# Kernel optimization log

Hardware: AMD Instinct MI355X
Metric: run time of the kernel (lower is better)

Reference implementation:

```python
import jax, jax.numpy as jnp
import numpy as np

D = 8
W = 256
NUM_FREQS = 10
NUM_FREQS_VIEWS = 4
SKIPS = (4,)
PE_DIM = 3 + 2 * 3 * NUM_FREQS        # 63
VE_DIM = 3 + 2 * 3 * NUM_FREQS_VIEWS  # 27
N_RAYS, N_SAMPLES = 4096, 64


def embed(x, num_freqs):
    # torch order: [x, sin(x*f0), cos(x*f0), sin(x*f1), cos(x*f1), ...]
    freqs = (2.0 ** jnp.arange(num_freqs)).astype(x.dtype)
    xf = x[..., None, :] * freqs[:, None]              # [..., F, 3]
    sc = jnp.stack([jnp.sin(xf), jnp.cos(xf)], axis=-2)  # [..., F, 2, 3]
    return jnp.concatenate([x, sc.reshape(*x.shape[:-1], num_freqs * 6)], -1)


def setup_inputs() -> dict:
    key = jax.random.key(0)
    ks = iter(jax.random.split(key, 32))
    inp = {}
    inp["input_pts"] = jax.random.normal(next(ks), (N_RAYS, N_SAMPLES, 3), jnp.float32)
    inp["input_views"] = jax.random.normal(next(ks), (N_RAYS, 3), jnp.float32)
    # pts MLP: layer 5 (index 5) takes W + PE_DIM due to skip after layer 4
    in_dims = [PE_DIM] + [(W + PE_DIM) if i in SKIPS else W for i in range(D - 1)]
    for i, d in enumerate(in_dims):
        inp[f"pts_w{i}"] = jax.random.normal(next(ks), (d, W), jnp.float32) / np.sqrt(d).astype(np.float32)
        inp[f"pts_b{i}"] = jnp.zeros((W,), jnp.float32)
    inp["views_w"] = jax.random.normal(next(ks), (VE_DIM + W, W // 2), jnp.float32) / np.sqrt(VE_DIM + W).astype(np.float32)
    inp["views_b"] = jnp.zeros((W // 2,), jnp.float32)
    inp["feat_w"] = jax.random.normal(next(ks), (W, W), jnp.float32) / np.sqrt(W).astype(np.float32)
    inp["feat_b"] = jnp.zeros((W,), jnp.float32)
    inp["alpha_w"] = jax.random.normal(next(ks), (W, 1), jnp.float32) / np.sqrt(W).astype(np.float32)
    inp["alpha_b"] = jnp.zeros((1,), jnp.float32)
    inp["rgb_w"] = jax.random.normal(next(ks), (W // 2, 3), jnp.float32) / np.sqrt(W // 2).astype(np.float32)
    inp["rgb_b"] = jnp.zeros((3,), jnp.float32)
    return inp


def reference(input_pts, input_views,
              pts_w0, pts_b0, pts_w1, pts_b1, pts_w2, pts_b2, pts_w3, pts_b3,
              pts_w4, pts_b4, pts_w5, pts_b5, pts_w6, pts_b6, pts_w7, pts_b7,
              views_w, views_b, feat_w, feat_b, alpha_w, alpha_b, rgb_w, rgb_b):
    pts_ws = [pts_w0, pts_w1, pts_w2, pts_w3, pts_w4, pts_w5, pts_w6, pts_w7]
    pts_bs = [pts_b0, pts_b1, pts_b2, pts_b3, pts_b4, pts_b5, pts_b6, pts_b7]
    R, S = input_pts.shape[0], input_pts.shape[1]
    ep = embed(input_pts, NUM_FREQS).reshape(-1, PE_DIM)            # [R*S, 63]
    ev = embed(input_views, NUM_FREQS_VIEWS)                        # [R, 27]
    ev = jnp.broadcast_to(ev[:, None, :], (R, S, VE_DIM)).reshape(-1, VE_DIM)
    h = ep
    for i in range(D):
        h = jax.nn.relu(h @ pts_ws[i] + pts_bs[i])
        if i in SKIPS:
            h = jnp.concatenate([ep, h], -1)
    alpha = h @ alpha_w + alpha_b                                    # [R*S, 1]
    feature = h @ feat_w + feat_b                                    # [R*S, W]
    h2 = jax.nn.relu(jnp.concatenate([feature, ev], -1) @ views_w + views_b)
    rgb = h2 @ rgb_w + rgb_b                                         # [R*S, 3]
    return jnp.concatenate([rgb, alpha], -1).reshape(R, S, 4)
```

## Files before the change

kernel.cpp:

```cpp
#include <hip/hip_runtime.h>

typedef _Float16 h16;
typedef __attribute__((ext_vector_type(8))) _Float16 half8;
typedef __attribute__((ext_vector_type(4))) _Float16 half4;
typedef __attribute__((ext_vector_type(4))) float f32x4;
typedef __attribute__((ext_vector_type(16))) float f32x16;

#define LDH 264
#define LDE 72

constexpr size_t OFF_P0 = 0;
constexpr size_t OFF_P1 = 16384;
constexpr size_t OFF_P2 = 81920;
constexpr size_t OFF_P3 = 147456;
constexpr size_t OFF_P4 = 212992;
constexpr size_t OFF_P5 = 278528;
constexpr size_t OFF_P6 = 360448;
constexpr size_t OFF_P7 = 425984;
constexpr size_t OFF_FEAT = 491520;
constexpr size_t OFF_VIEWS = 557056;

__device__ __forceinline__ f32x16 mfma32(half8 a, half8 b, f32x16 c) {
  return __builtin_amdgcn_mfma_f32_32x32x16_f16(a, b, c, 0, 0, 0);
}

__device__ __forceinline__ half8 ldfrag(const h16* __restrict__ base, int frag, int l) {
  return *(const half8*)(base + (size_t)frag * 512 + (size_t)l * 8);
}

__global__ void convw_kernel(const float* __restrict__ src, h16* __restrict__ dst,
                             int Ksrc, int N, int Kp, int p, int npad, int rot) {
  int t = blockIdx.x * 256 + threadIdx.x;
  int nfrags = (Kp >> 4) * (N >> 5);
  int frag = t >> 6;
  if (frag >= nfrags) return;
  int l = t & 63;
  int ntiles = N >> 5;
  int kt = frag / ntiles;
  int nt = frag - kt * ntiles;
  int col = nt * 32 + (l & 31);
  int kbase = kt * 16 + (l >> 5) * 8;
  half8 v;
#pragma unroll
  for (int j = 0; j < 8; ++j) {
    int pr = kbase + j + rot;
    if (pr >= Kp) pr -= Kp;
    float x = 0.f;
    if (pr < p) {
      x = src[(size_t)pr * N + col];
    } else if (pr >= p + npad) {
      int r = pr - npad;
      if (r < Ksrc) x = src[(size_t)r * N + col];
    }
    v[j] = (h16)x;
  }
  *(half8*)(dst + (size_t)frag * 512 + (size_t)l * 8) = v;
}

struct Params {
  const float* pts;
  const float* views;
  const h16* wf;
  const float* pb[8];
  const float* views_b;
  const float* feat_b;
  const float* alpha_w;
  const float* alpha_b;
  const float* rgb_w;
  const float* rgb_b;
  float* out;
};

template <bool RELU>
__device__ __forceinline__ void epi(const f32x16& a0, const f32x16& a1,
                                    const float* __restrict__ bias,
                                    h16* __restrict__ Y, int w, int l, int lr) {
#pragma unroll
  for (int mt = 0; mt < 2; ++mt) {
    const f32x16& A = mt ? a1 : a0;
    int row = mt * 32 + lr;
#pragma unroll
    for (int g = 0; g < 4; ++g) {
      int n0 = w * 32 + g * 8 + ((l >> 5) * 4);
      f32x4 bv = *(const f32x4*)(bias + n0);
      half4 pk;
#pragma unroll
      for (int i = 0; i < 4; ++i) {
        float v = A[g * 4 + i] + bv[i];
        if (RELU) v = fmaxf(v, 0.f);
        pk[i] = (h16)v;
      }
      *(half4*)(Y + (size_t)row * LDH + n0) = pk;
    }
  }
}

template <bool RELU, bool EXTEP>
__device__ __forceinline__ void layer256(
    const h16* __restrict__ X, const h16* __restrict__ EPb, h16* __restrict__ Y,
    const h16* __restrict__ wcur, const h16* __restrict__ wnext,
    int nstride, int nbase, const float* __restrict__ bias,
    half8 (&bf)[8], half8 (&bt)[8], int w, int l, int lr, int lko) {
#pragma unroll
  for (int j = 0; j < 8; ++j) bt[j] = ldfrag(wcur, (8 + j) * 8 + w, l);
  half8 bep[4];
  f32x16 acc0 = (f32x16)0.f, acc1 = (f32x16)0.f;
#pragma unroll
  for (int kt = 0; kt < 16; ++kt) {
    half8 a = *(const half8*)(X + (size_t)lr * LDH + kt * 16 + lko);
    half8 b = kt < 8 ? bf[kt] : bt[kt - 8];
    acc0 = mfma32(b, a, acc0);
    if (EXTEP && kt == 7) {
#pragma unroll
      for (int j = 0; j < 4; ++j) bep[j] = ldfrag(wcur, (16 + j) * 8 + w, l);
    }
  }
  if (EXTEP) {
#pragma unroll
    for (int j = 0; j < 4; ++j) {
      half8 a = *(const half8*)(EPb + (size_t)lr * LDE + j * 16 + lko);
      acc0 = mfma32(bep[j], a, acc0);
    }
  }
#pragma unroll
  for (int kt = 0; kt < 16; ++kt) {
    half8 a = *(const half8*)(X + (size_t)(32 + lr) * LDH + kt * 16 + lko);
    half8 b = kt < 8 ? bf[kt] : bt[kt - 8];
    acc1 = mfma32(b, a, acc1);
    if (kt < 8) bf[kt] = ldfrag(wnext, kt * nstride + nbase, l);
  }
  if (EXTEP) {
#pragma unroll
    for (int j = 0; j < 4; ++j) {
      half8 a = *(const half8*)(EPb + (size_t)(32 + lr) * LDE + j * 16 + lko);
      acc1 = mfma32(bep[j], a, acc1);
    }
  }
  epi<RELU>(acc0, acc1, bias, Y, w, l, lr);
  __syncthreads();
}

__global__ __launch_bounds__(512, 4) void nerf_kernel(Params P) {
  __shared__ __align__(16) h16 ep[64 * LDE];
  __shared__ __align__(16) h16 h0[64 * LDH];
  __shared__ __align__(16) h16 h1[64 * LDH];
  __shared__ __align__(16) h16 evp[32];

  const int tid = threadIdx.x;
  const int w = tid >> 6, l = tid & 63;
  const int lr = l & 31;
  const int lko = (l >> 5) * 8;
  const int ray = blockIdx.x;
  const h16* wf = P.wf;

  half8 bt[8];
#pragma unroll
  for (int j = 0; j < 4; ++j) bt[j] = ldfrag(wf + OFF_P0, j * 8 + w, l);

  {
    const int s = tid >> 3, q = tid & 7;
    const float* ps = P.pts + ((size_t)ray * 64 + s) * 3;
    const float x0 = ps[0], x1 = ps[1], x2 = ps[2];
    half8 v;
#pragma unroll
    for (int j = 0; j < 8; ++j) {
      int p = q * 8 + j;
      float val;
      if (p < 3) {
        val = p == 0 ? x0 : (p == 1 ? x1 : x2);
      } else if (p < 63) {
        int t = p - 3;
        int f = t / 6, rem = t % 6, d = rem % 3;
        float x = (d == 0 ? x0 : (d == 1 ? x1 : x2)) * (float)(1 << f);
        val = (rem < 3) ? sinf(x) : cosf(x);
      } else {
        val = 0.f;
      }
      v[j] = (h16)val;
    }
    *(half8*)(ep + (size_t)s * LDE + q * 8) = v;
  }
  if (tid < 32) {
    const int idx = tid;
    float v = 0.f;
    if (idx < 27) {
      if (idx < 3) {
        v = P.views[(size_t)ray * 3 + idx];
      } else {
        const int f = (idx - 3) / 6, rem = (idx - 3) % 6, d = rem % 3;
        const float x = P.views[(size_t)ray * 3 + d] * (float)(1 << f);
        v = (rem < 3) ? sinf(x) : cosf(x);
      }
    }
    evp[idx] = (h16)v;
  }
  __syncthreads();

  half8 bf[8];

  {
    f32x16 acc0 = (f32x16)0.f, acc1 = (f32x16)0.f;
#pragma unroll
    for (int kt = 0; kt < 4; ++kt) {
      half8 a = *(const half8*)(ep + (size_t)lr * LDE + kt * 16 + lko);
      acc0 = mfma32(bt[kt], a, acc0);
    }
#pragma unroll
    for (int kt = 0; kt < 4; ++kt) {
      half8 a = *(const half8*)(ep + (size_t)(32 + lr) * LDE + kt * 16 + lko);
      acc1 = mfma32(bt[kt], a, acc1);
    }
#pragma unroll
    for (int j = 0; j < 8; ++j) bf[j] = ldfrag(wf + OFF_P1, j * 8 + w, l);
    epi<true>(acc0, acc1, P.pb[0], h0, w, l, lr);
    __syncthreads();
  }

  layer256<true, false>(h0, ep, h1, wf + OFF_P1, wf + OFF_P2, 8, w, P.pb[1], bf, bt, w, l, lr, lko);
  layer256<true, false>(h1, ep, h0, wf + OFF_P2, wf + OFF_P3, 8, w, P.pb[2], bf, bt, w, l, lr, lko);
  layer256<true, false>(h0, ep, h1, wf + OFF_P3, wf + OFF_P4, 8, w, P.pb[3], bf, bt, w, l, lr, lko);
  layer256<true, false>(h1, ep, h0, wf + OFF_P4, wf + OFF_P5, 8, w, P.pb[4], bf, bt, w, l, lr, lko);
  layer256<true, true>(h0, ep, h1, wf + OFF_P5, wf + OFF_P6, 8, w, P.pb[5], bf, bt, w, l, lr, lko);
  layer256<true, false>(h1, ep, h0, wf + OFF_P6, wf + OFF_P7, 8, w, P.pb[6], bf, bt, w, l, lr, lko);
  layer256<true, false>(h0, ep, h1, wf + OFF_P7, wf + OFF_FEAT, 8, w, P.pb[7], bf, bt, w, l, lr, lko);

  float alpha_reg;
  {
    const int s = tid >> 3, q = tid & 7;
    float sum = 0.f;
#pragma unroll
    for (int j = 0; j < 4; ++j) {
      half8 hv = *(const half8*)(h1 + (size_t)s * LDH + q * 32 + j * 8);
#pragma unroll
      for (int i = 0; i < 8; ++i)
        sum += (float)hv[i] * P.alpha_w[q * 32 + j * 8 + i];
    }
    sum += __shfl_xor(sum, 1);
    sum += __shfl_xor(sum, 2);
    sum += __shfl_xor(sum, 4);
    alpha_reg = sum + P.alpha_b[0];
  }

  layer256<false, false>(h1, ep, h0, wf + OFF_FEAT, wf + OFF_VIEWS, 4, (w >> 1),
                         P.feat_b, bf, bt, w, l, lr, lko);

  {
    const int r = w & 1, c = w >> 1;
    const h16* wV = wf + OFF_VIEWS;
#pragma unroll
    for (int j = 0; j < 8; ++j) bt[j] = ldfrag(wV, (8 + j) * 4 + c, l);
    half8 bev[2];
    f32x16 acc = (f32x16)0.f;
#pragma unroll
    for (int kt = 0; kt < 16; ++kt) {
      half8 a = *(const half8*)(h0 + (size_t)(r * 32 + lr) * LDH + kt * 16 + lko);
      half8 b = kt < 8 ? bf[kt] : bt[kt - 8];
      acc = mfma32(b, a, acc);
      if (kt == 7) {
        bev[0] = ldfrag(wV, 16 * 4 + c, l);
        bev[1] = ldfrag(wV, 17 * 4 + c, l);
      }
    }
#pragma unroll
    for (int j = 0; j < 2; ++j) {
      half8 a = *(const half8*)(evp + j * 16 + lko);
      acc = mfma32(bev[j], a, acc);
    }
    const int row = r * 32 + lr;
#pragma unroll
    for (int g = 0; g < 4; ++g) {
      int n0 = c * 32 + g * 8 + ((l >> 5) * 4);
      f32x4 bv = *(const f32x4*)(P.views_b + n0);
      half4 pk;
#pragma unroll
      for (int i = 0; i < 4; ++i)
        pk[i] = (h16)fmaxf(acc[g * 4 + i] + bv[i], 0.f);
      *(half4*)(h1 + (size_t)row * LDH + n0) = pk;
    }
    __syncthreads();
  }

  {
    const int s = tid >> 3, q = tid & 7;
    float r0 = 0.f, r1 = 0.f, r2 = 0.f;
#pragma unroll
    for (int j = 0; j < 2; ++j) {
      half8 hv = *(const half8*)(h1 + (size_t)s * LDH + q * 16 + j * 8);
#pragma unroll
      for (int i = 0; i < 8; ++i) {
        const int kk = q * 16 + j * 8 + i;
        const float f = (float)hv[i];
        r0 += f * P.rgb_w[kk * 3 + 0];
        r1 += f * P.rgb_w[kk * 3 + 1];
        r2 += f * P.rgb_w[kk * 3 + 2];
      }
    }
    r0 += __shfl_xor(r0, 1); r0 += __shfl_xor(r0, 2); r0 += __shfl_xor(r0, 4);
    r1 += __shfl_xor(r1, 1); r1 += __shfl_xor(r1, 2); r1 += __shfl_xor(r1, 4);
    r2 += __shfl_xor(r2, 1); r2 += __shfl_xor(r2, 2); r2 += __shfl_xor(r2, 4);
    if (q == 0) {
      float4 o;
      o.x = r0 + P.rgb_b[0];
      o.y = r1 + P.rgb_b[1];
      o.z = r2 + P.rgb_b[2];
      o.w = alpha_reg;
      *(float4*)(P.out + ((size_t)ray * 64 + s) * 4) = o;
    }
  }
}

extern "C" void kernel_launch(void* const* d_in, const int* in_sizes, int n_in,
                              void* d_out, int out_size, void* d_ws, size_t ws_size,
                              hipStream_t stream) {
  h16* wsw = (h16*)d_ws;
  auto conv = [&](int idx, int Ksrc, int N, int Kp, int p, int npad, int rot, size_t off) {
    int nfrags = (Kp / 16) * (N / 32);
    int total = nfrags * 64;
    convw_kernel<<<(total + 255) / 256, 256, 0, stream>>>(
        (const float*)d_in[idx], wsw + off, Ksrc, N, Kp, p, npad, rot);
  };
  conv(2, 63, 256, 64, 63, 1, 0, OFF_P0);
  conv(4, 256, 256, 256, 256, 0, 0, OFF_P1);
  conv(6, 256, 256, 256, 256, 0, 0, OFF_P2);
  conv(8, 256, 256, 256, 256, 0, 0, OFF_P3);
  conv(10, 256, 256, 256, 256, 0, 0, OFF_P4);
  conv(12, 319, 256, 320, 63, 1, 64, OFF_P5);
  conv(14, 256, 256, 256, 256, 0, 0, OFF_P6);
  conv(16, 256, 256, 256, 256, 0, 0, OFF_P7);
  conv(20, 256, 256, 256, 256, 0, 0, OFF_FEAT);
  conv(18, 283, 128, 288, 283, 5, 0, OFF_VIEWS);

  Params P;
  P.pts = (const float*)d_in[0];
  P.views = (const float*)d_in[1];
  P.wf = wsw;
  for (int i = 0; i < 8; ++i) P.pb[i] = (const float*)d_in[3 + 2 * i];
  P.views_b = (const float*)d_in[19];
  P.feat_b = (const float*)d_in[21];
  P.alpha_w = (const float*)d_in[22];
  P.alpha_b = (const float*)d_in[23];
  P.rgb_w = (const float*)d_in[24];
  P.rgb_b = (const float*)d_in[25];
  P.out = (float*)d_out;

  nerf_kernel<<<4096, 512, 0, stream>>>(P);
}
```

Measured before the change: 388.3 us.

## Process two rays per block with 2x2 warp tiles and fragment-layout activations

Each block now handles 128 samples (two rays) instead of 64, and each wave computes a 64x64 output tile (two row tiles by two column tiles). Every weight fragment loaded from global memory is therefore reused across twice as many rows, halving per-sample weight traffic. Activations are stored in shared memory in MFMA fragment order rather than padded row-major, so A-operand reads become contiguous 16-byte loads. Weight loads use a rolling 4-deep register prefetch that crosses into the next layer. The cost is about twice the LDS per block and more accumulator registers, with launch bounds lowered to 2 blocks per SM, so occupancy drops.

```diff
diff --git a/kernel.cpp b/kernel.cpp
--- a/kernel.cpp
+++ b/kernel.cpp
@@ -5,9 +5,6 @@
 typedef __attribute__((ext_vector_type(4))) _Float16 half4;
 typedef __attribute__((ext_vector_type(4))) float f32x4;
 typedef __attribute__((ext_vector_type(16))) float f32x16;
-
-#define LDH 264
-#define LDE 72
 
 constexpr size_t OFF_P0 = 0;
 constexpr size_t OFF_P1 = 16384;
@@ -23,9 +20,11 @@
 __device__ __forceinline__ f32x16 mfma32(half8 a, half8 b, f32x16 c) {
   return __builtin_amdgcn_mfma_f32_32x32x16_f16(a, b, c, 0, 0, 0);
 }
-
 __device__ __forceinline__ half8 ldfrag(const h16* __restrict__ base, int frag, int l) {
   return *(const half8*)(base + (size_t)frag * 512 + (size_t)l * 8);
+}
+__device__ __forceinline__ half8 ldsfrag(const h16* __restrict__ base, int frag, int l) {
+  return *(const half8*)(base + frag * 512 + l * 8);
 }
 
 __global__ void convw_kernel(const float* __restrict__ src, h16* __restrict__ dst,
@@ -72,99 +71,89 @@
 };
 
 template <bool RELU>
-__device__ __forceinline__ void epi(const f32x16& a0, const f32x16& a1,
-                                    const float* __restrict__ bias,
-                                    h16* __restrict__ Y, int w, int l, int lr) {
-#pragma unroll
-  for (int mt = 0; mt < 2; ++mt) {
-    const f32x16& A = mt ? a1 : a0;
-    int row = mt * 32 + lr;
-#pragma unroll
-    for (int g = 0; g < 4; ++g) {
-      int n0 = w * 32 + g * 8 + ((l >> 5) * 4);
-      f32x4 bv = *(const f32x4*)(bias + n0);
-      half4 pk;
-#pragma unroll
-      for (int i = 0; i < 4; ++i) {
-        float v = A[g * 4 + i] + bv[i];
-        if (RELU) v = fmaxf(v, 0.f);
-        pk[i] = (h16)v;
-      }
-      *(half4*)(Y + (size_t)row * LDH + n0) = pk;
-    }
-  }
-}
-
-template <bool RELU, bool EXTEP>
-__device__ __forceinline__ void layer256(
+__device__ __forceinline__ void epiW(h16* __restrict__ Y, const f32x16& A,
+                                     int rt, int ct, const float* __restrict__ bias,
+                                     int lr, int lh) {
+#pragma unroll
+  for (int g = 0; g < 4; ++g) {
+    int col0 = ct * 32 + g * 8 + lh * 4;
+    f32x4 bv = *(const f32x4*)(bias + col0);
+    half4 pk;
+#pragma unroll
+    for (int i = 0; i < 4; ++i) {
+      float v = A[g * 4 + i] + bv[i];
+      if (RELU) v = fmaxf(v, 0.f);
+      pk[i] = (h16)v;
+    }
+    *(half4*)(Y + (rt * 16 + ct * 2 + (g >> 1)) * 512 + ((g & 1) * 32 + lr) * 8 + lh * 4) = pk;
+  }
+}
+
+template <int KTTOT, int XSTRIDE, bool RELU, bool EXTEP>
+__device__ __forceinline__ void layerT(
     const h16* __restrict__ X, const h16* __restrict__ EPb, h16* __restrict__ Y,
     const h16* __restrict__ wcur, const h16* __restrict__ wnext,
-    int nstride, int nbase, const float* __restrict__ bias,
-    half8 (&bf)[8], half8 (&bt)[8], int w, int l, int lr, int lko) {
-#pragma unroll
-  for (int j = 0; j < 8; ++j) bt[j] = ldfrag(wcur, (8 + j) * 8 + w, l);
-  half8 bep[4];
-  f32x16 acc0 = (f32x16)0.f, acc1 = (f32x16)0.f;
-#pragma unroll
-  for (int kt = 0; kt < 16; ++kt) {
-    half8 a = *(const half8*)(X + (size_t)lr * LDH + kt * 16 + lko);
-    half8 b = kt < 8 ? bf[kt] : bt[kt - 8];
-    acc0 = mfma32(b, a, acc0);
-    if (EXTEP && kt == 7) {
-#pragma unroll
-      for (int j = 0; j < 4; ++j) bep[j] = ldfrag(wcur, (16 + j) * 8 + w, l);
-    }
-  }
-  if (EXTEP) {
-#pragma unroll
-    for (int j = 0; j < 4; ++j) {
-      half8 a = *(const half8*)(EPb + (size_t)lr * LDE + j * 16 + lko);
-      acc0 = mfma32(bep[j], a, acc0);
-    }
-  }
-#pragma unroll
-  for (int kt = 0; kt < 16; ++kt) {
-    half8 a = *(const half8*)(X + (size_t)(32 + lr) * LDH + kt * 16 + lko);
-    half8 b = kt < 8 ? bf[kt] : bt[kt - 8];
-    acc1 = mfma32(b, a, acc1);
-    if (kt < 8) bf[kt] = ldfrag(wnext, kt * nstride + nbase, l);
-  }
-  if (EXTEP) {
-#pragma unroll
-    for (int j = 0; j < 4; ++j) {
-      half8 a = *(const half8*)(EPb + (size_t)(32 + lr) * LDE + j * 16 + lko);
-      acc1 = mfma32(bep[j], a, acc1);
-    }
-  }
-  epi<RELU>(acc0, acc1, bias, Y, w, l, lr);
+    int nstride, int nbA, int nbB, const float* __restrict__ bias,
+    half8 (&rA)[4], half8 (&rB)[4], int rp, int ctA, int ctB, int l) {
+  const int lr = l & 31, lh = l >> 5;
+  f32x16 a00 = (f32x16)0.f, a01 = (f32x16)0.f, a10 = (f32x16)0.f, a11 = (f32x16)0.f;
+#pragma unroll
+  for (int kt = 0; kt < KTTOT; ++kt) {
+    half8 x0, x1;
+    if (!EXTEP || kt < 16) {
+      x0 = ldsfrag(X, (2 * rp) * XSTRIDE + kt, l);
+      x1 = ldsfrag(X, (2 * rp + 1) * XSTRIDE + kt, l);
+    } else {
+      x0 = ldsfrag(EPb, (2 * rp) * 4 + (kt - 16), l);
+      x1 = ldsfrag(EPb, (2 * rp + 1) * 4 + (kt - 16), l);
+    }
+    half8 bA = rA[kt & 3], bB = rB[kt & 3];
+    if (kt + 4 < KTTOT) {
+      rA[kt & 3] = ldfrag(wcur, (kt + 4) * 8 + ctA, l);
+      rB[kt & 3] = ldfrag(wcur, (kt + 4) * 8 + ctB, l);
+    } else {
+      rA[kt & 3] = ldfrag(wnext, (kt + 4 - KTTOT) * nstride + nbA, l);
+      rB[kt & 3] = ldfrag(wnext, (kt + 4 - KTTOT) * nstride + nbB, l);
+    }
+    a00 = mfma32(bA, x0, a00);
+    a01 = mfma32(bB, x0, a01);
+    a10 = mfma32(bA, x1, a10);
+    a11 = mfma32(bB, x1, a11);
+  }
+  epiW<RELU>(Y, a00, 2 * rp, ctA, bias, lr, lh);
+  epiW<RELU>(Y, a01, 2 * rp, ctB, bias, lr, lh);
+  epiW<RELU>(Y, a10, 2 * rp + 1, ctA, bias, lr, lh);
+  epiW<RELU>(Y, a11, 2 * rp + 1, ctB, bias, lr, lh);
   __syncthreads();
 }
 
-__global__ __launch_bounds__(512, 4) void nerf_kernel(Params P) {
-  __shared__ __align__(16) h16 ep[64 * LDE];
-  __shared__ __align__(16) h16 h0[64 * LDH];
-  __shared__ __align__(16) h16 h1[64 * LDH];
-  __shared__ __align__(16) h16 evp[32];
+__global__ __launch_bounds__(512, 2) void nerf_kernel(Params P) {
+  __shared__ __align__(16) h16 ep[16 * 512];
+  __shared__ __align__(16) h16 h0[64 * 512];
+  __shared__ __align__(16) h16 h1[64 * 512];
+  __shared__ __align__(16) h16 evp[64];
 
   const int tid = threadIdx.x;
   const int w = tid >> 6, l = tid & 63;
-  const int lr = l & 31;
-  const int lko = (l >> 5) * 8;
-  const int ray = blockIdx.x;
+  const int rp = w & 1, cp = w >> 1;
+  const int ctA = 2 * cp, ctB = 2 * cp + 1;
   const h16* wf = P.wf;
 
-  half8 bt[8];
-#pragma unroll
-  for (int j = 0; j < 4; ++j) bt[j] = ldfrag(wf + OFF_P0, j * 8 + w, l);
+  half8 rA[4], rB[4];
+#pragma unroll
+  for (int j = 0; j < 4; ++j) {
+    rA[j] = ldfrag(wf + OFF_P0, j * 8 + ctA, l);
+    rB[j] = ldfrag(wf + OFF_P0, j * 8 + ctB, l);
+  }
 
   {
-    const int s = tid >> 3, q = tid & 7;
-    const float* ps = P.pts + ((size_t)ray * 64 + s) * 3;
+    const int s = tid >> 2, q = tid & 3;
+    const float* ps = P.pts + ((size_t)blockIdx.x * 128 + s) * 3;
     const float x0 = ps[0], x1 = ps[1], x2 = ps[2];
-    half8 v;
-#pragma unroll
-    for (int j = 0; j < 8; ++j) {
-      int p = q * 8 + j;
+    half8 v0, v1;
+#pragma unroll
+    for (int jj = 0; jj < 16; ++jj) {
+      int p = q * 16 + jj;
       float val;
       if (p < 3) {
         val = p == 0 ? x0 : (p == 1 ? x1 : x2);
@@ -176,135 +165,110 @@
       } else {
         val = 0.f;
       }
-      v[j] = (h16)val;
-    }
-    *(half8*)(ep + (size_t)s * LDE + q * 8) = v;
-  }
-  if (tid < 32) {
-    const int idx = tid;
+      if (jj < 8) v0[jj] = (h16)val; else v1[jj - 8] = (h16)val;
+    }
+    int fr = (s >> 5) * 4 + q;
+    *(half8*)(ep + fr * 512 + (s & 31) * 8) = v0;
+    *(half8*)(ep + fr * 512 + (32 + (s & 31)) * 8) = v1;
+  }
+  if (tid < 64) {
+    const int r = tid >> 5, idx = tid & 31;
     float v = 0.f;
     if (idx < 27) {
       if (idx < 3) {
-        v = P.views[(size_t)ray * 3 + idx];
+        v = P.views[((size_t)blockIdx.x * 2 + r) * 3 + idx];
       } else {
         const int f = (idx - 3) / 6, rem = (idx - 3) % 6, d = rem % 3;
-        const float x = P.views[(size_t)ray * 3 + d] * (float)(1 << f);
+        const float x = P.views[((size_t)blockIdx.x * 2 + r) * 3 + d] * (float)(1 << f);
         v = (rem < 3) ? sinf(x) : cosf(x);
       }
     }
-    evp[idx] = (h16)v;
+    evp[r * 32 + idx] = (h16)v;
   }
   __syncthreads();
 
-  half8 bf[8];
-
-  {
-    f32x16 acc0 = (f32x16)0.f, acc1 = (f32x16)0.f;
-#pragma unroll
-    for (int kt = 0; kt < 4; ++kt) {
-      half8 a = *(const half8*)(ep + (size_t)lr * LDE + kt * 16 + lko);
-      acc0 = mfma32(bt[kt], a, acc0);
-    }
-#pragma unroll
-    for (int kt = 0; kt < 4; ++kt) {
-      half8 a = *(const half8*)(ep + (size_t)(32 + lr) * LDE + kt * 16 + lko);
-      acc1 = mfma32(bt[kt], a, acc1);
-    }
-#pragma unroll
-    for (int j = 0; j < 8; ++j) bf[j] = ldfrag(wf + OFF_P1, j * 8 + w, l);
-    epi<true>(acc0, acc1, P.pb[0], h0, w, l, lr);
-    __syncthreads();
-  }
-
-  layer256<true, false>(h0, ep, h1, wf + OFF_P1, wf + OFF_P2, 8, w, P.pb[1], bf, bt, w, l, lr, lko);
-  layer256<true, false>(h1, ep, h0, wf + OFF_P2, wf + OFF_P3, 8, w, P.pb[2], bf, bt, w, l, lr, lko);
-  layer256<true, false>(h0, ep, h1, wf + OFF_P3, wf + OFF_P4, 8, w, P.pb[3], bf, bt, w, l, lr, lko);
-  layer256<true, false>(h1, ep, h0, wf + OFF_P4, wf + OFF_P5, 8, w, P.pb[4], bf, bt, w, l, lr, lko);
-  layer256<true, true>(h0, ep, h1, wf + OFF_P5, wf + OFF_P6, 8, w, P.pb[5], bf, bt, w, l, lr, lko);
-  layer256<true, false>(h1, ep, h0, wf + OFF_P6, wf + OFF_P7, 8, w, P.pb[6], bf, bt, w, l, lr, lko);
-  layer256<true, false>(h0, ep, h1, wf + OFF_P7, wf + OFF_FEAT, 8, w, P.pb[7], bf, bt, w, l, lr, lko);
+  layerT<4, 4, true, false>(ep, ep, h0, wf + OFF_P0, wf + OFF_P1, 8, ctA, ctB, P.pb[0], rA, rB, rp, ctA, ctB, l);
+  layerT<16, 16, true, false>(h0, ep, h1, wf + OFF_P1, wf + OFF_P2, 8, ctA, ctB, P.pb[1], rA, rB, rp, ctA, ctB, l);
+  layerT<16, 16, true, false>(h1, ep, h0, wf + OFF_P2, wf + OFF_P3, 8, ctA, ctB, P.pb[2], rA, rB, rp, ctA, ctB, l);
+  layerT<16, 16, true, false>(h0, ep, h1, wf + OFF_P3, wf + OFF_P4, 8, ctA, ctB, P.pb[3], rA, rB, rp, ctA, ctB, l);
+  layerT<16, 16, true, false>(h1, ep, h0, wf + OFF_P4, wf + OFF_P5, 8, ctA, ctB, P.pb[4], rA, rB, rp, ctA, ctB, l);
+  layerT<20, 16, true, true>(h0, ep, h1, wf + OFF_P5, wf + OFF_P6, 8, ctA, ctB, P.pb[5], rA, rB, rp, ctA, ctB, l);
+  layerT<16, 16, true, false>(h1, ep, h0, wf + OFF_P6, wf + OFF_P7, 8, ctA, ctB, P.pb[6], rA, rB, rp, ctA, ctB, l);
+  layerT<16, 16, true, false>(h0, ep, h1, wf + OFF_P7, wf + OFF_FEAT, 8, ctA, ctB, P.pb[7], rA, rB, rp, ctA, ctB, l);
 
   float alpha_reg;
   {
-    const int s = tid >> 3, q = tid & 7;
+    const int s = tid >> 2, q = tid & 3;
     float sum = 0.f;
 #pragma unroll
-    for (int j = 0; j < 4; ++j) {
-      half8 hv = *(const half8*)(h1 + (size_t)s * LDH + q * 32 + j * 8);
-#pragma unroll
-      for (int i = 0; i < 8; ++i)
-        sum += (float)hv[i] * P.alpha_w[q * 32 + j * 8 + i];
+    for (int j = 0; j < 8; ++j) {
+      int k0 = q * 64 + j * 8;
+      half8 hv = *(const half8*)(h1 + ((s >> 5) * 16 + (k0 >> 4)) * 512 +
+                                 ((s & 31) + 32 * ((k0 >> 3) & 1)) * 8);
+      f32x4 w0 = *(const f32x4*)(P.alpha_w + k0);
+      f32x4 w1 = *(const f32x4*)(P.alpha_w + k0 + 4);
+      sum += (float)hv[0] * w0[0] + (float)hv[1] * w0[1] + (float)hv[2] * w0[2] + (float)hv[3] * w0[3];
+      sum += (float)hv[4] * w1[0] + (float)hv[5] * w1[1] + (float)hv[6] * w1[2] + (float)hv[7] * w1[3];
     }
     sum += __shfl_xor(sum, 1);
     sum += __shfl_xor(sum, 2);
-    sum += __shfl_xor(sum, 4);
     alpha_reg = sum + P.alpha_b[0];
   }
 
-  layer256<false, false>(h1, ep, h0, wf + OFF_FEAT, wf + OFF_VIEWS, 4, (w >> 1),
-                         P.feat_b, bf, bt, w, l, lr, lko);
+  layerT<16, 16, false, false>(h1, ep, h0, wf + OFF_FEAT, wf + OFF_VIEWS, 4,
+                               2 * (w >> 2), 2 * (w >> 2) + 1, P.feat_b,
+                               rA, rB, rp, ctA, ctB, l);
 
   {
-    const int r = w & 1, c = w >> 1;
+    const int rt = w & 3, cv = w >> 2;
+    const int vA = 2 * cv, vB = 2 * cv + 1;
+    const int lr = l & 31, lh = l >> 5;
     const h16* wV = wf + OFF_VIEWS;
-#pragma unroll
-    for (int j = 0; j < 8; ++j) bt[j] = ldfrag(wV, (8 + j) * 4 + c, l);
-    half8 bev[2];
-    f32x16 acc = (f32x16)0.f;
-#pragma unroll
-    for (int kt = 0; kt < 16; ++kt) {
-      half8 a = *(const half8*)(h0 + (size_t)(r * 32 + lr) * LDH + kt * 16 + lko);
-      half8 b = kt < 8 ? bf[kt] : bt[kt - 8];
-      acc = mfma32(b, a, acc);
-      if (kt == 7) {
-        bev[0] = ldfrag(wV, 16 * 4 + c, l);
-        bev[1] = ldfrag(wV, 17 * 4 + c, l);
+    f32x16 accA = (f32x16)0.f, accB = (f32x16)0.f;
+#pragma unroll
+    for (int kt = 0; kt < 18; ++kt) {
+      half8 x;
+      if (kt < 16) x = ldsfrag(h0, rt * 16 + kt, l);
+      else x = *(const half8*)(evp + (rt >> 1) * 32 + (kt - 16) * 16 + lh * 8);
+      half8 bA = rA[kt & 3], bB = rB[kt & 3];
+      if (kt + 4 < 18) {
+        rA[kt & 3] = ldfrag(wV, (kt + 4) * 4 + vA, l);
+        rB[kt & 3] = ldfrag(wV, (kt + 4) * 4 + vB, l);
       }
-    }
-#pragma unroll
-    for (int j = 0; j < 2; ++j) {
-      half8 a = *(const half8*)(evp + j * 16 + lko);
-      acc = mfma32(bev[j], a, acc);
-    }
-    const int row = r * 32 + lr;
-#pragma unroll
-    for (int g = 0; g < 4; ++g) {
-      int n0 = c * 32 + g * 8 + ((l >> 5) * 4);
-      f32x4 bv = *(const f32x4*)(P.views_b + n0);
-      half4 pk;
-#pragma unroll
-      for (int i = 0; i < 4; ++i)
-        pk[i] = (h16)fmaxf(acc[g * 4 + i] + bv[i], 0.f);
-      *(half4*)(h1 + (size_t)row * LDH + n0) = pk;
-    }
+      accA = mfma32(bA, x, accA);
+      accB = mfma32(bB, x, accB);
+    }
+    epiW<true>(h1, accA, rt, vA, P.views_b, lr, lh);
+    epiW<true>(h1, accB, rt, vB, P.views_b, lr, lh);
     __syncthreads();
   }
 
   {
-    const int s = tid >> 3, q = tid & 7;
+    const int s = tid >> 2, q = tid & 3;
     float r0 = 0.f, r1 = 0.f, r2 = 0.f;
 #pragma unroll
-    for (int j = 0; j < 2; ++j) {
-      half8 hv = *(const half8*)(h1 + (size_t)s * LDH + q * 16 + j * 8);
+    for (int j = 0; j < 4; ++j) {
+      int k0 = q * 32 + j * 8;
+      half8 hv = *(const half8*)(h1 + ((s >> 5) * 16 + (k0 >> 4)) * 512 +
+                                 ((s & 31) + 32 * ((k0 >> 3) & 1)) * 8);
 #pragma unroll
       for (int i = 0; i < 8; ++i) {
-        const int kk = q * 16 + j * 8 + i;
         const float f = (float)hv[i];
-        r0 += f * P.rgb_w[kk * 3 + 0];
-        r1 += f * P.rgb_w[kk * 3 + 1];
-        r2 += f * P.rgb_w[kk * 3 + 2];
+        r0 += f * P.rgb_w[(k0 + i) * 3 + 0];
+        r1 += f * P.rgb_w[(k0 + i) * 3 + 1];
+        r2 += f * P.rgb_w[(k0 + i) * 3 + 2];
       }
     }
-    r0 += __shfl_xor(r0, 1); r0 += __shfl_xor(r0, 2); r0 += __shfl_xor(r0, 4);
-    r1 += __shfl_xor(r1, 1); r1 += __shfl_xor(r1, 2); r1 += __shfl_xor(r1, 4);
-    r2 += __shfl_xor(r2, 1); r2 += __shfl_xor(r2, 2); r2 += __shfl_xor(r2, 4);
+    r0 += __shfl_xor(r0, 1); r0 += __shfl_xor(r0, 2);
+    r1 += __shfl_xor(r1, 1); r1 += __shfl_xor(r1, 2);
+    r2 += __shfl_xor(r2, 1); r2 += __shfl_xor(r2, 2);
     if (q == 0) {
       float4 o;
       o.x = r0 + P.rgb_b[0];
       o.y = r1 + P.rgb_b[1];
       o.z = r2 + P.rgb_b[2];
       o.w = alpha_reg;
-      *(float4*)(P.out + ((size_t)ray * 64 + s) * 4) = o;
+      *(float4*)(P.out + ((size_t)blockIdx.x * 128 + s) * 4) = o;
     }
   }
 }
@@ -343,5 +307,5 @@
   P.rgb_b = (const float*)d_in[25];
   P.out = (float*)d_out;
 
-  nerf_kernel<<<4096, 512, 0, stream>>>(P);
-}
+  nerf_kernel<<<2048, 512, 0, stream>>>(P);
+}
```

Result: slower. 432.9 us (+11.5%).
